# Kernel optimization log

Measured on AMD Instinct MI355X. Metric: run time of the kernel, lower is better.

The kernel has to match this reference:

```python
import jax, jax.numpy as jnp
import numpy as np

DIM = 1024

def setup_inputs() -> dict:
    key = jax.random.key(0)
    ks = jax.random.split(key, 7)
    s = 1.0 / np.sqrt(DIM)
    x = jax.random.normal(ks[0], (8, 2048, DIM), dtype=jnp.float32)
    Wq = jax.random.uniform(ks[1], (DIM, DIM), jnp.float32, -s, s)
    bq = jax.random.uniform(ks[2], (DIM,), jnp.float32, -s, s)
    Wk = jax.random.uniform(ks[3], (DIM, DIM), jnp.float32, -s, s)
    bk = jax.random.uniform(ks[4], (DIM,), jnp.float32, -s, s)
    Wv = jax.random.uniform(ks[5], (DIM, DIM), jnp.float32, -s, s)
    bv = jax.random.uniform(ks[6], (DIM,), jnp.float32, -s, s)
    return {"x": x, "Wq": Wq, "bq": bq, "Wk": Wk, "bk": bk, "Wv": Wv, "bv": bv}

def reference(x, Wq, bq, Wk, bk, Wv, bv):
    # nn.Linear: y = x @ W.T + b
    q = jnp.einsum('bsd,ed->bse', x, Wq) + bq  # [B,S,D]
    k = jnp.einsum('bsd,ed->bse', x, Wk) + bk
    v = jnp.einsum('bsd,ed->bse', x, Wv) + bv
    scores = jnp.einsum('bqd,bkd->bqk', q, k) / jnp.sqrt(jnp.float32(DIM))
    attn = jax.nn.softmax(scores, axis=-1)
    return jnp.einsum('bqk,bkd->bqd', attn, v)
```

## Files before the change

kernel.cpp:

```cpp
#include <hip/hip_runtime.h>

#define DIM 1024
#define SEQ 2048

typedef __attribute__((ext_vector_type(8))) short bf16x8;
typedef __attribute__((ext_vector_type(16))) float f32x16;
typedef __attribute__((ext_vector_type(4))) unsigned short us4;
typedef __attribute__((ext_vector_type(4))) _Float16 h4;

__device__ __forceinline__ unsigned short f2bf(float f) {
    union { float f; unsigned int u; } v; v.f = f;
    unsigned int r = (v.u + 0x7FFFu + ((v.u >> 16) & 1u)) >> 16;
    return (unsigned short)r;
}

#define GLOAD(gp, lp) __builtin_amdgcn_global_load_lds( \
    (const __attribute__((address_space(1))) unsigned int*)(gp), \
    (__attribute__((address_space(3))) unsigned int*)(lp), 16, 0, 0)

#define MFMA32(a, b, c) __builtin_amdgcn_mfma_f32_32x32x16_bf16((a), (b), (c), 0, 0, 0)

__global__ __launch_bounds__(256) void cast_f32_bf16(const float* __restrict__ src,
                                                     unsigned short* __restrict__ dst, int n) {
    int i = (blockIdx.x * 256 + threadIdx.x) * 8;
    if (i >= n) return;
    float4 a = *(const float4*)(src + i);
    float4 b = *(const float4*)(src + i + 4);
    us4 lo = { f2bf(a.x), f2bf(a.y), f2bf(a.z), f2bf(a.w) };
    us4 hi = { f2bf(b.x), f2bf(b.y), f2bf(b.z), f2bf(b.w) };
    *(us4*)(dst + i) = lo;
    *(us4*)(dst + i + 4) = hi;
}

__device__ __forceinline__ void gemm256_core(
    const unsigned short* __restrict__ A, const unsigned short* __restrict__ B,
    int lda, int ldb, int K, char* smem, f32x16 acc[4][2])
{
    const int tid = threadIdx.x;
    const int lane = tid & 63;
    const int wm = (tid >> 6) >> 2;
    const int wn = (tid >> 6) & 3;
    const int l31 = lane & 31, lhi = lane >> 5;

    const int schunk = ((tid & 3) ^ ((tid >> 3) & 3)) * 8;
    const unsigned short* paw = A + (size_t)(tid >> 2) * lda + schunk;
    const unsigned short* pbw = B + (size_t)(tid >> 2) * ldb + schunk;
    const int doff = tid * 16;

    const int fsw = (l31 >> 1) & 3;
    const int abase = (wm * 128 + l31) * 64;
    const int bbase = 16384 + (wn * 64 + l31) * 64;
    int csw[4];
#pragma unroll
    for (int c = 0; c < 4; c++) csw[c] = ((c ^ fsw)) * 16;

    const int NT = K >> 5;

#define STAGE32(bb, kt) do { \
    GLOAD(paw + (kt),                      smem + (bb) + doff); \
    GLOAD(paw + (kt) + (size_t)128 * lda,  smem + (bb) + 8192 + doff); \
    GLOAD(pbw + (kt),                      smem + (bb) + 16384 + doff); \
    GLOAD(pbw + (kt) + (size_t)128 * ldb,  smem + (bb) + 24576 + doff); \
} while (0)

    STAGE32(0, 0);

    for (int T = 0; T < NT; ++T) {
        asm volatile("s_waitcnt vmcnt(0)" ::: "memory");
        __builtin_amdgcn_s_barrier();

        if (T + 1 < NT) STAGE32(((T + 1) & 1) * 32768, (size_t)(T + 1) * 32);

        const char* db = smem + (T & 1) * 32768;
        bf16x8 a0[4], a1[4], b0[2], b1[2];
#pragma unroll
        for (int mi = 0; mi < 4; mi++) {
            a0[mi] = *(const bf16x8*)(db + abase + mi * 2048 + csw[lhi]);
            a1[mi] = *(const bf16x8*)(db + abase + mi * 2048 + csw[2 + lhi]);
        }
#pragma unroll
        for (int nj = 0; nj < 2; nj++) {
            b0[nj] = *(const bf16x8*)(db + bbase + nj * 2048 + csw[lhi]);
            b1[nj] = *(const bf16x8*)(db + bbase + nj * 2048 + csw[2 + lhi]);
        }

        __builtin_amdgcn_s_setprio(1);
#pragma unroll
        for (int mi = 0; mi < 4; mi++)
#pragma unroll
            for (int nj = 0; nj < 2; nj++)
                acc[mi][nj] = MFMA32(a0[mi], b0[nj], acc[mi][nj]);
#pragma unroll
        for (int mi = 0; mi < 4; mi++)
#pragma unroll
            for (int nj = 0; nj < 2; nj++)
                acc[mi][nj] = MFMA32(a1[mi], b1[nj], acc[mi][nj]);
        __builtin_amdgcn_s_setprio(0);
    }
#undef STAGE32
}

#define ACC_INIT() \
    f32x16 acc[4][2]; \
    _Pragma("unroll") for (int i = 0; i < 4; i++) \
    _Pragma("unroll") for (int jj = 0; jj < 2; jj++) acc[i][jj] = (f32x16){}; \


template<int BZ>
__global__ __launch_bounds__(512, 2) void gemm_qkv_t(
    const unsigned short* __restrict__ xb, const unsigned short* __restrict__ w,
    const float* __restrict__ bias, unsigned short* __restrict__ C)
{
    extern __shared__ char smem[];
    const int bid = blockIdx.x;
    const int lb = (bid & 7) * 32 + (bid >> 3);
    const int m0 = (lb >> 2) * 256, n0 = (lb & 3) * 256;
    ACC_INIT();
    gemm256_core(xb + (size_t)m0 * DIM, w + (size_t)n0 * DIM, DIM, DIM, DIM, smem, acc);
    const int lane = threadIdx.x & 63, wid = threadIdx.x >> 6;
    const int wm = wid >> 2, wn = wid & 3;
    const int l31 = lane & 31, lhi = lane >> 5;
#pragma unroll
    for (int mi = 0; mi < 4; mi++)
#pragma unroll
        for (int nj = 0; nj < 2; nj++) {
            const int col = n0 + wn * 64 + nj * 32 + l31;
            const float bcol = bias[col];
            if (BZ < 2) {
                const float scale = (BZ == 0) ? 0.03125f : 1.0f;
#pragma unroll
                for (int r = 0; r < 16; r++) {
                    const int row = m0 + wm * 128 + mi * 32 + (r & 3) + 8 * (r >> 2) + 4 * lhi;
                    C[(size_t)row * DIM + col] = f2bf((acc[mi][nj][r] + bcol) * scale);
                }
            } else {
#pragma unroll
                for (int r4 = 0; r4 < 4; r4++) {
                    const int s0 = m0 + wm * 128 + mi * 32 + 8 * r4 + 4 * lhi;
                    const int b = s0 >> 11, s = s0 & 2047;
                    us4 pk = { f2bf(acc[mi][nj][r4 * 4] + bcol),
                               f2bf(acc[mi][nj][r4 * 4 + 1] + bcol),
                               f2bf(acc[mi][nj][r4 * 4 + 2] + bcol),
                               f2bf(acc[mi][nj][r4 * 4 + 3] + bcol) };
                    *(us4*)&C[((size_t)b << 21) + ((size_t)col << 11) + s] = pk;
                }
            }
        }
}

__global__ __launch_bounds__(512, 2) void gemm_qk(
    const unsigned short* __restrict__ qb, const unsigned short* __restrict__ kb,
    unsigned short* __restrict__ sb)
{
    extern __shared__ char smem[];
    const int bid = blockIdx.x;
    const int lb = (bid & 7) * 64 + (bid >> 3);
    const int b = lb >> 6;
    const int r0 = lb & 63;
    const int m0 = (r0 >> 3) * 256, n0 = (r0 & 7) * 256;
    ACC_INIT();
    gemm256_core(qb + ((size_t)b * SEQ + m0) * DIM, kb + ((size_t)b * SEQ + n0) * DIM,
                 DIM, DIM, DIM, smem, acc);
    const int lane = threadIdx.x & 63, wid = threadIdx.x >> 6;
    const int wm = wid >> 2, wn = wid & 3;
    const int l31 = lane & 31, lhi = lane >> 5;
    _Float16* sh = (_Float16*)sb + (size_t)b * SEQ * SEQ;
#pragma unroll
    for (int mi = 0; mi < 4; mi++)
#pragma unroll
        for (int nj = 0; nj < 2; nj++) {
            const int col = n0 + wn * 64 + nj * 32 + l31;
#pragma unroll
            for (int r = 0; r < 16; r++) {
                const int row = m0 + wm * 128 + mi * 32 + (r & 3) + 8 * (r >> 2) + 4 * lhi;
                sh[(size_t)row * SEQ + col] = (_Float16)acc[mi][nj][r];
            }
        }
}

__global__ __launch_bounds__(256) void softmax_p(unsigned short* __restrict__ sb)
{
    const int lane = threadIdx.x & 63, wid = threadIdx.x >> 6;
    const size_t row = (size_t)blockIdx.x * 4 + wid;
    unsigned short* rp = sb + row * SEQ;
    float v[32];
#pragma unroll
    for (int j = 0; j < 8; j++) {
        h4 h = *(const h4*)(rp + (j * 64 + lane) * 4);
#pragma unroll
        for (int e = 0; e < 4; e++) v[j * 4 + e] = (float)h[e];
    }
    float m = -1e30f;
#pragma unroll
    for (int i = 0; i < 32; i++) m = fmaxf(m, v[i]);
#pragma unroll
    for (int msk = 1; msk <= 32; msk <<= 1) m = fmaxf(m, __shfl_xor(m, msk, 64));
    float s = 0.f;
#pragma unroll
    for (int i = 0; i < 32; i++) { v[i] = __expf(v[i] - m); s += v[i]; }
#pragma unroll
    for (int msk = 1; msk <= 32; msk <<= 1) s += __shfl_xor(s, msk, 64);
    float inv = 1.0f / s;
#pragma unroll
    for (int j = 0; j < 8; j++) {
        us4 pu = { f2bf(v[j * 4] * inv), f2bf(v[j * 4 + 1] * inv),
                   f2bf(v[j * 4 + 2] * inv), f2bf(v[j * 4 + 3] * inv) };
        *(us4*)(rp + (j * 64 + lane) * 4) = pu;
    }
}

__global__ __launch_bounds__(512, 2) void gemm_pv(
    const unsigned short* __restrict__ pb, const unsigned short* __restrict__ vt,
    float* __restrict__ out)
{
    extern __shared__ char smem[];
    const int bid = blockIdx.x;
    const int lb = (bid & 7) * 32 + (bid >> 3);
    const int b = lb >> 5;
    const int r0 = lb & 31;
    const int m0 = (r0 >> 2) * 256, n0 = (r0 & 3) * 256;
    ACC_INIT();
    gemm256_core(pb + ((size_t)b * SEQ + m0) * SEQ, vt + ((size_t)b * DIM + n0) * SEQ,
                 SEQ, SEQ, SEQ, smem, acc);
    const int lane = threadIdx.x & 63, wid = threadIdx.x >> 6;
    const int wm = wid >> 2, wn = wid & 3;
    const int l31 = lane & 31, lhi = lane >> 5;
    float* O = out + (size_t)b * SEQ * DIM;
#pragma unroll
    for (int mi = 0; mi < 4; mi++)
#pragma unroll
        for (int nj = 0; nj < 2; nj++) {
            const int col = n0 + wn * 64 + nj * 32 + l31;
#pragma unroll
            for (int r = 0; r < 16; r++) {
                const int row = m0 + wm * 128 + mi * 32 + (r & 3) + 8 * (r >> 2) + 4 * lhi;
                O[(size_t)row * DIM + col] = acc[mi][nj][r];
            }
        }
}

extern "C" void kernel_launch(void* const* d_in, const int* in_sizes, int n_in,
                              void* d_out, int out_size, void* d_ws, size_t ws_size,
                              hipStream_t stream) {
    const float* x  = (const float*)d_in[0];
    const float* Wq = (const float*)d_in[1];
    const float* bq = (const float*)d_in[2];
    const float* Wk = (const float*)d_in[3];
    const float* bk = (const float*)d_in[4];
    const float* Wv = (const float*)d_in[5];
    const float* bv = (const float*)d_in[6];
    float* out = (float*)d_out;
    char* ws = (char*)d_ws;

    unsigned short* xb = (unsigned short*)(ws);
    unsigned short* wb = (unsigned short*)(ws + 33554432);
    unsigned short* qb = (unsigned short*)(ws + 39845888);
    unsigned short* kb = (unsigned short*)(ws + 73400320);
    unsigned short* vt = (unsigned short*)(ws + 106954752);
    unsigned short* sb = (unsigned short*)(ws + 140509184);

    cast_f32_bf16<<<dim3(8192), 256, 0, stream>>>(x, xb, 16777216);
    cast_f32_bf16<<<dim3(512), 256, 0, stream>>>(Wq, wb, 1048576);
    cast_f32_bf16<<<dim3(512), 256, 0, stream>>>(Wk, wb + 1048576, 1048576);
    cast_f32_bf16<<<dim3(512), 256, 0, stream>>>(Wv, wb + 2097152, 1048576);

    hipFuncSetAttribute((const void*)gemm_qkv_t<0>, hipFuncAttributeMaxDynamicSharedMemorySize, 65536);
    hipFuncSetAttribute((const void*)gemm_qkv_t<1>, hipFuncAttributeMaxDynamicSharedMemorySize, 65536);
    hipFuncSetAttribute((const void*)gemm_qkv_t<2>, hipFuncAttributeMaxDynamicSharedMemorySize, 65536);
    hipFuncSetAttribute((const void*)gemm_qk,  hipFuncAttributeMaxDynamicSharedMemorySize, 65536);
    hipFuncSetAttribute((const void*)gemm_pv,  hipFuncAttributeMaxDynamicSharedMemorySize, 65536);

    gemm_qkv_t<0><<<dim3(256), 512, 65536, stream>>>(xb, wb,           bq, qb);
    gemm_qkv_t<1><<<dim3(256), 512, 65536, stream>>>(xb, wb + 1048576, bk, kb);
    gemm_qkv_t<2><<<dim3(256), 512, 65536, stream>>>(xb, wb + 2097152, bv, vt);
    gemm_qk<<<dim3(512), 512, 65536, stream>>>(qb, kb, sb);
    softmax_p<<<dim3(4096), 256, 0, stream>>>(sb);
    gemm_pv<<<dim3(256), 512, 65536, stream>>>(sb, vt, out);
}
```

Measured before the change: 313.1 us.

## Shrink GEMM tiles to 128x128 with 4 waves and fuse QKV launches

Switches every GEMM from 256x256 tiles (8 waves, 64KB dynamic LDS) to 128x128 tiles (4 waves, 32KB static LDS), which quadruples the block count. It also merges the three Q/K/V projection launches into a single kernel that picks the weight, bias and output from the block index. More, smaller blocks are meant to fill the 256 CUs better and cut launch overhead. In exchange, each tile gets half the operand reuse per loaded byte, so global and L2 traffic per FLOP roughly doubles.

```diff
diff --git a/kernel.cpp b/kernel.cpp
--- a/kernel.cpp
+++ b/kernel.cpp
@@ -32,14 +32,14 @@
     *(us4*)(dst + i + 4) = hi;
 }
 
-__device__ __forceinline__ void gemm256_core(
+__device__ __forceinline__ void gemm128_core(
     const unsigned short* __restrict__ A, const unsigned short* __restrict__ B,
-    int lda, int ldb, int K, char* smem, f32x16 acc[4][2])
+    int lda, int ldb, int K, char* smem, f32x16 acc[2][2])
 {
     const int tid = threadIdx.x;
     const int lane = tid & 63;
-    const int wm = (tid >> 6) >> 2;
-    const int wn = (tid >> 6) & 3;
+    const int wm = (tid >> 6) >> 1;
+    const int wn = (tid >> 6) & 1;
     const int l31 = lane & 31, lhi = lane >> 5;
 
     const int schunk = ((tid & 3) ^ ((tid >> 3) & 3)) * 8;
@@ -48,33 +48,33 @@
     const int doff = tid * 16;
 
     const int fsw = (l31 >> 1) & 3;
-    const int abase = (wm * 128 + l31) * 64;
-    const int bbase = 16384 + (wn * 64 + l31) * 64;
+    const int abase = (wm * 64 + l31) * 64;
+    const int bbase = 8192 + (wn * 64 + l31) * 64;
     int csw[4];
 #pragma unroll
-    for (int c = 0; c < 4; c++) csw[c] = ((c ^ fsw)) * 16;
+    for (int c = 0; c < 4; c++) csw[c] = (c ^ fsw) * 16;
 
     const int NT = K >> 5;
 
-#define STAGE32(bb, kt) do { \
-    GLOAD(paw + (kt),                      smem + (bb) + doff); \
-    GLOAD(paw + (kt) + (size_t)128 * lda,  smem + (bb) + 8192 + doff); \
-    GLOAD(pbw + (kt),                      smem + (bb) + 16384 + doff); \
-    GLOAD(pbw + (kt) + (size_t)128 * ldb,  smem + (bb) + 24576 + doff); \
+#define STAGE128(bb, kt) do { \
+    GLOAD(paw + (kt),                     smem + (bb) + doff); \
+    GLOAD(paw + (kt) + (size_t)64 * lda,  smem + (bb) + 4096 + doff); \
+    GLOAD(pbw + (kt),                     smem + (bb) + 8192 + doff); \
+    GLOAD(pbw + (kt) + (size_t)64 * ldb,  smem + (bb) + 12288 + doff); \
 } while (0)
 
-    STAGE32(0, 0);
+    STAGE128(0, 0);
 
     for (int T = 0; T < NT; ++T) {
         asm volatile("s_waitcnt vmcnt(0)" ::: "memory");
         __builtin_amdgcn_s_barrier();
 
-        if (T + 1 < NT) STAGE32(((T + 1) & 1) * 32768, (size_t)(T + 1) * 32);
-
-        const char* db = smem + (T & 1) * 32768;
-        bf16x8 a0[4], a1[4], b0[2], b1[2];
-#pragma unroll
-        for (int mi = 0; mi < 4; mi++) {
+        if (T + 1 < NT) STAGE128(((T + 1) & 1) * 16384, (size_t)(T + 1) * 32);
+
+        const char* db = smem + (T & 1) * 16384;
+        bf16x8 a0[2], a1[2], b0[2], b1[2];
+#pragma unroll
+        for (int mi = 0; mi < 2; mi++) {
             a0[mi] = *(const bf16x8*)(db + abase + mi * 2048 + csw[lhi]);
             a1[mi] = *(const bf16x8*)(db + abase + mi * 2048 + csw[2 + lhi]);
         }
@@ -86,93 +86,98 @@
 
         __builtin_amdgcn_s_setprio(1);
 #pragma unroll
-        for (int mi = 0; mi < 4; mi++)
+        for (int mi = 0; mi < 2; mi++)
 #pragma unroll
             for (int nj = 0; nj < 2; nj++)
                 acc[mi][nj] = MFMA32(a0[mi], b0[nj], acc[mi][nj]);
 #pragma unroll
-        for (int mi = 0; mi < 4; mi++)
+        for (int mi = 0; mi < 2; mi++)
 #pragma unroll
             for (int nj = 0; nj < 2; nj++)
                 acc[mi][nj] = MFMA32(a1[mi], b1[nj], acc[mi][nj]);
         __builtin_amdgcn_s_setprio(0);
     }
-#undef STAGE32
+#undef STAGE128
 }
 
 #define ACC_INIT() \
-    f32x16 acc[4][2]; \
-    _Pragma("unroll") for (int i = 0; i < 4; i++) \
+    f32x16 acc[2][2]; \
+    _Pragma("unroll") for (int i = 0; i < 2; i++) \
     _Pragma("unroll") for (int jj = 0; jj < 2; jj++) acc[i][jj] = (f32x16){}; \
 
 
-template<int BZ>
-__global__ __launch_bounds__(512, 2) void gemm_qkv_t(
-    const unsigned short* __restrict__ xb, const unsigned short* __restrict__ w,
-    const float* __restrict__ bias, unsigned short* __restrict__ C)
-{
-    extern __shared__ char smem[];
+__global__ __launch_bounds__(256) void gemm_qkv(
+    const unsigned short* __restrict__ xb, const unsigned short* __restrict__ wb,
+    const float* __restrict__ bq, const float* __restrict__ bk, const float* __restrict__ bv,
+    unsigned short* __restrict__ qb, unsigned short* __restrict__ kb, unsigned short* __restrict__ vt)
+{
+    __shared__ char smem[32768];
     const int bid = blockIdx.x;
-    const int lb = (bid & 7) * 32 + (bid >> 3);
-    const int m0 = (lb >> 2) * 256, n0 = (lb & 3) * 256;
+    const int lb = (bid & 7) * 384 + (bid >> 3);
+    const int bz = lb >> 10;
+    const int r0 = lb & 1023;
+    const int m0 = (r0 >> 3) * 128, n0 = (r0 & 7) * 128;
+    const float* bias = (bz == 0) ? bq : ((bz == 1) ? bk : bv);
     ACC_INIT();
-    gemm256_core(xb + (size_t)m0 * DIM, w + (size_t)n0 * DIM, DIM, DIM, DIM, smem, acc);
-    const int lane = threadIdx.x & 63, wid = threadIdx.x >> 6;
-    const int wm = wid >> 2, wn = wid & 3;
-    const int l31 = lane & 31, lhi = lane >> 5;
-#pragma unroll
-    for (int mi = 0; mi < 4; mi++)
+    gemm128_core(xb + (size_t)m0 * DIM, wb + (size_t)bz * DIM * DIM + (size_t)n0 * DIM,
+                 DIM, DIM, DIM, smem, acc);
+    const int lane = threadIdx.x & 63, wid = threadIdx.x >> 6;
+    const int wm = wid >> 1, wn = wid & 1;
+    const int l31 = lane & 31, lhi = lane >> 5;
+#pragma unroll
+    for (int mi = 0; mi < 2; mi++)
 #pragma unroll
         for (int nj = 0; nj < 2; nj++) {
             const int col = n0 + wn * 64 + nj * 32 + l31;
             const float bcol = bias[col];
-            if (BZ < 2) {
-                const float scale = (BZ == 0) ? 0.03125f : 1.0f;
+            if (bz < 2) {
+                unsigned short* C = (bz == 0) ? qb : kb;
+                const float scale = (bz == 0) ? 0.03125f : 1.0f;
 #pragma unroll
                 for (int r = 0; r < 16; r++) {
-                    const int row = m0 + wm * 128 + mi * 32 + (r & 3) + 8 * (r >> 2) + 4 * lhi;
+                    const int row = m0 + wm * 64 + mi * 32 + (r & 3) + 8 * (r >> 2) + 4 * lhi;
                     C[(size_t)row * DIM + col] = f2bf((acc[mi][nj][r] + bcol) * scale);
                 }
             } else {
 #pragma unroll
                 for (int r4 = 0; r4 < 4; r4++) {
-                    const int s0 = m0 + wm * 128 + mi * 32 + 8 * r4 + 4 * lhi;
+                    const int s0 = m0 + wm * 64 + mi * 32 + 8 * r4 + 4 * lhi;
                     const int b = s0 >> 11, s = s0 & 2047;
                     us4 pk = { f2bf(acc[mi][nj][r4 * 4] + bcol),
                                f2bf(acc[mi][nj][r4 * 4 + 1] + bcol),
                                f2bf(acc[mi][nj][r4 * 4 + 2] + bcol),
                                f2bf(acc[mi][nj][r4 * 4 + 3] + bcol) };
-                    *(us4*)&C[((size_t)b << 21) + ((size_t)col << 11) + s] = pk;
+                    *(us4*)&vt[((size_t)b << 21) + ((size_t)col << 11) + s] = pk;
                 }
             }
         }
 }
 
-__global__ __launch_bounds__(512, 2) void gemm_qk(
+__global__ __launch_bounds__(256) void gemm_qk(
     const unsigned short* __restrict__ qb, const unsigned short* __restrict__ kb,
     unsigned short* __restrict__ sb)
 {
-    extern __shared__ char smem[];
+    __shared__ char smem[32768];
     const int bid = blockIdx.x;
-    const int lb = (bid & 7) * 64 + (bid >> 3);
-    const int b = lb >> 6;
-    const int r0 = lb & 63;
-    const int m0 = (r0 >> 3) * 256, n0 = (r0 & 7) * 256;
+    const int lb = (bid & 7) * 256 + (bid >> 3);
+    const int b = lb >> 8;
+    const int r0 = lb & 255;
+    const int m0 = (r0 >> 4) * 128, n0 = (r0 & 15) * 128;
     ACC_INIT();
-    gemm256_core(qb + ((size_t)b * SEQ + m0) * DIM, kb + ((size_t)b * SEQ + n0) * DIM,
+    gemm128_core(qb + ((size_t)b * SEQ + m0) * DIM, kb + ((size_t)b * SEQ + n0) * DIM,
                  DIM, DIM, DIM, smem, acc);
     const int lane = threadIdx.x & 63, wid = threadIdx.x >> 6;
-    const int wm = wid >> 2, wn = wid & 3;
+    const int wm = wid >> 1, wn = wid & 1;
     const int l31 = lane & 31, lhi = lane >> 5;
     _Float16* sh = (_Float16*)sb + (size_t)b * SEQ * SEQ;
 #pragma unroll
-    for (int mi = 0; mi < 4; mi++)
+    for (int mi = 0; mi < 2; mi++)
 #pragma unroll
         for (int nj = 0; nj < 2; nj++) {
             const int col = n0 + wn * 64 + nj * 32 + l31;
 #pragma unroll
             for (int r = 0; r < 16; r++) {
-                const int row = m0 + wm * 128 + mi * 32 + (r & 3) + 8 * (r >> 2) + 4 * lhi;
+                const int row = m0 + wm * 64 + mi * 32 + (r & 3) + 8 * (r >> 2) + 4 * lhi;
                 sh[(size_t)row * SEQ + col] = (_Float16)acc[mi][nj][r];
             }
         }
@@ -209,31 +214,31 @@
     }
 }
 
-__global__ __launch_bounds__(512, 2) void gemm_pv(
+__global__ __launch_bounds__(256) void gemm_pv(
     const unsigned short* __restrict__ pb, const unsigned short* __restrict__ vt,
     float* __restrict__ out)
 {
-    extern __shared__ char smem[];
+    __shared__ char smem[32768];
     const int bid = blockIdx.x;
-    const int lb = (bid & 7) * 32 + (bid >> 3);
-    const int b = lb >> 5;
-    const int r0 = lb & 31;
-    const int m0 = (r0 >> 2) * 256, n0 = (r0 & 3) * 256;
+    const int lb = (bid & 7) * 128 + (bid >> 3);
+    const int b = lb >> 7;
+    const int r0 = lb & 127;
+    const int m0 = (r0 >> 3) * 128, n0 = (r0 & 7) * 128;
     ACC_INIT();
-    gemm256_core(pb + ((size_t)b * SEQ + m0) * SEQ, vt + ((size_t)b * DIM + n0) * SEQ,
+    gemm128_core(pb + ((size_t)b * SEQ + m0) * SEQ, vt + ((size_t)b * DIM + n0) * SEQ,
                  SEQ, SEQ, SEQ, smem, acc);
     const int lane = threadIdx.x & 63, wid = threadIdx.x >> 6;
-    const int wm = wid >> 2, wn = wid & 3;
+    const int wm = wid >> 1, wn = wid & 1;
     const int l31 = lane & 31, lhi = lane >> 5;
     float* O = out + (size_t)b * SEQ * DIM;
 #pragma unroll
-    for (int mi = 0; mi < 4; mi++)
+    for (int mi = 0; mi < 2; mi++)
 #pragma unroll
         for (int nj = 0; nj < 2; nj++) {
             const int col = n0 + wn * 64 + nj * 32 + l31;
 #pragma unroll
             for (int r = 0; r < 16; r++) {
-                const int row = m0 + wm * 128 + mi * 32 + (r & 3) + 8 * (r >> 2) + 4 * lhi;
+                const int row = m0 + wm * 64 + mi * 32 + (r & 3) + 8 * (r >> 2) + 4 * lhi;
                 O[(size_t)row * DIM + col] = acc[mi][nj][r];
             }
         }
@@ -264,16 +269,8 @@
     cast_f32_bf16<<<dim3(512), 256, 0, stream>>>(Wk, wb + 1048576, 1048576);
     cast_f32_bf16<<<dim3(512), 256, 0, stream>>>(Wv, wb + 2097152, 1048576);
 
-    hipFuncSetAttribute((const void*)gemm_qkv_t<0>, hipFuncAttributeMaxDynamicSharedMemorySize, 65536);
-    hipFuncSetAttribute((const void*)gemm_qkv_t<1>, hipFuncAttributeMaxDynamicSharedMemorySize, 65536);
-    hipFuncSetAttribute((const void*)gemm_qkv_t<2>, hipFuncAttributeMaxDynamicSharedMemorySize, 65536);
-    hipFuncSetAttribute((const void*)gemm_qk,  hipFuncAttributeMaxDynamicSharedMemorySize, 65536);
-    hipFuncSetAttribute((const void*)gemm_pv,  hipFuncAttributeMaxDynamicSharedMemorySize, 65536);
-
-    gemm_qkv_t<0><<<dim3(256), 512, 65536, stream>>>(xb, wb,           bq, qb);
-    gemm_qkv_t<1><<<dim3(256), 512, 65536, stream>>>(xb, wb + 1048576, bk, kb);
-    gemm_qkv_t<2><<<dim3(256), 512, 65536, stream>>>(xb, wb + 2097152, bv, vt);
-    gemm_qk<<<dim3(512), 512, 65536, stream>>>(qb, kb, sb);
+    gemm_qkv<<<dim3(3072), 256, 0, stream>>>(xb, wb, bq, bk, bv, qb, kb, vt);
+    gemm_qk<<<dim3(2048), 256, 0, stream>>>(qb, kb, sb);
     softmax_p<<<dim3(4096), 256, 0, stream>>>(sb);
-    gemm_pv<<<dim3(256), 512, 65536, stream>>>(sb, vt, out);
-}
+    gemm_pv<<<dim3(1024), 256, 0, stream>>>(sb, vt, out);
+}
```

New measurement: 351.3 us. +12.2%, slower.
